# Kernel optimization log

Measured on AMD Instinct MI355X. Metric: run time of the kernel, lower is better.

## Reference

```python
import jax, jax.numpy as jnp
import numpy as np

# ---- module config (matches init_kwargs) ----
OGFH, OGFW = 256, 704
DOWNSAMPLE = 8
FH, FW = OGFH // DOWNSAMPLE, OGFW // DOWNSAMPLE   # 32, 88
DBOUND = (4.0, 45.0, 1.0)
D = int((DBOUND[1] - DBOUND[0]) / DBOUND[2])      # 41 depth bins
CAMC = 64
XB = (-50.0, 50.0, 0.5)    # lateral  -> nx = 200
YB = (-10.0, 10.0, 20.0)   # vertical -> ny = 1
ZB = (0.0, 50.0, 0.25)     # depth    -> nz = 200
NX = np.array([int((b[1] - b[0]) / b[2]) for b in (XB, YB, ZB)])  # [200, 1, 200]
DX = np.array([b[2] for b in (XB, YB, ZB)], dtype=np.float32)
BX = np.array([b[0] + b[2] / 2.0 for b in (XB, YB, ZB)], dtype=np.float32)


def make_frustum():
    # matches create_frustum_1camera: [D, fH, fW, 3] of (u, v, depth)
    ds = jnp.broadcast_to(
        jnp.arange(DBOUND[0], DBOUND[1], DBOUND[2], dtype=jnp.float32)[:, None, None],
        (D, FH, FW))
    xs = jnp.broadcast_to(
        jnp.linspace(0.0, OGFW - 1, FW, dtype=jnp.float32)[None, None, :], (D, FH, FW))
    ys = jnp.broadcast_to(
        jnp.linspace(0.0, OGFH - 1, FH, dtype=jnp.float32)[None, :, None], (D, FH, FW))
    return jnp.stack((xs, ys, ds), -1)


def setup_inputs() -> dict:
    key = jax.random.key(0)
    B = 4
    # depthnet output: first D channels = depth logits, next CAMC = context feats
    x = jax.random.normal(key, (B, D + CAMC, FH, FW), dtype=jnp.float32)
    fx = fy = 520.0
    K = jnp.array([[fx, 0.0, OGFW / 2.0],
                   [0.0, fy, OGFH / 2.0],
                   [0.0, 0.0, 1.0]], dtype=jnp.float32)
    intrins = jnp.broadcast_to(K, (B, 3, 3))
    post_rots = jnp.broadcast_to(jnp.eye(3, dtype=jnp.float32), (B, 3, 3))
    post_trans = jnp.zeros((B, 3), dtype=jnp.float32)
    return {"x": x, "intrins": intrins, "post_rots": post_rots, "post_trans": post_trans}


def _forward(x, intrins, post_rots, post_trans):
    B = x.shape[0]
    frustum = make_frustum()                                                     # [D,H,W,3]
    # ---- get_geometry ----
    pts = frustum[None] - post_trans[:, None, None, None, :]                     # [B,D,H,W,3]
    pts = jnp.einsum('bij,bdhwj->bdhwi', jnp.linalg.inv(post_rots), pts)
    pts = jnp.concatenate([pts[..., :2] * pts[..., 2:3], pts[..., 2:3]], -1)     # un-normalize
    geom = jnp.einsum('bij,bdhwj->bdhwi', jnp.linalg.inv(intrins), pts)          # [B,D,H,W,3]
    # ---- lift: depth softmax (x) context features ----
    depth = jax.nn.softmax(x[:, :D], axis=1)                                     # [B,D,H,W]
    feat = x[:, D:D + CAMC]                                                      # [B,C,H,W]
    vol = depth[:, None] * feat[:, :, None]                                      # [B,C,D,H,W]
    vol = jnp.transpose(vol, (0, 2, 3, 4, 1))                                    # [B,D,H,W,C]
    # ---- voxel_splat (sort+cumsum trick == segmented sum) ----
    Nprime = B * D * FH * FW
    feats = vol.reshape(Nprime, CAMC)
    # torch .long() truncates toward zero -> astype(int32)
    coords = ((geom - (BX - DX / 2.0)) / DX).astype(jnp.int32).reshape(Nprime, 3)
    bix = jnp.repeat(jnp.arange(B, dtype=jnp.int32), Nprime // B)
    kept = ((coords[:, 0] >= 0) & (coords[:, 0] < int(NX[0])) &
            (coords[:, 1] >= 0) & (coords[:, 1] < int(NX[1])) &
            (coords[:, 2] >= 0) & (coords[:, 2] < int(NX[2])))
    nseg = int(NX[0] * NX[1] * NX[2]) * B
    ranks = (coords[:, 0] * (int(NX[1]) * int(NX[2]) * B)
             + coords[:, 1] * (int(NX[2]) * B)
             + coords[:, 2] * B + bix)
    ranks = jnp.where(kept, ranks, nseg)  # dump bucket for dropped points
    pooled = jax.ops.segment_sum(jnp.where(kept[:, None], feats, 0.0), ranks,
                                 num_segments=nseg + 1)[:nseg]
    final = pooled.reshape(int(NX[0]), int(NX[1]), int(NX[2]), B, CAMC)          # [x,y,z,B,C]
    final = jnp.transpose(final, (3, 4, 1, 2, 0))                                # [B,C,ny,nz,nx]
    # torch.cat(final.unbind(dim=2), 1): collapse ny into channels (y-major)
    final = jnp.transpose(final, (0, 2, 1, 3, 4)).reshape(
        B, CAMC * int(NX[1]), int(NX[2]), int(NX[0]))                            # [B,C,200,200]
    return final


def reference(x, intrins, post_rots, post_trans):
    return _forward(x, intrins, post_rots, post_trans)
```

## Files before the change

kernel.cpp:

```cpp
#include <hip/hip_runtime.h>
#include <math.h>

#define DD   41
#define FHh  32
#define FWw  88
#define CC   64
#define CH   32
#define CG8  8
#define NXx  200
#define NZz  200
#define NCH  (DD + CC)
#define PLANE ((size_t)FHh * FWw)
#define NE   (DD * FWw)
#define DCAP 4
#define OVCAP 4096

__global__ __launch_bounds__(256) void lss_colpool(
    const float* __restrict__ x,
    const float* __restrict__ intrins,
    const float* __restrict__ post_rots,
    const float* __restrict__ post_trans,
    float* __restrict__ P, int* __restrict__ V,
    int* __restrict__ rowcnt8, int* __restrict__ ovcnt,
    float* __restrict__ out, int out_quads)
{
    __shared__ float Wt[DD][FHh + 1];
    __shared__ float F4s[FHh][36];
    __shared__ float Mi[18];
    __shared__ float pm[8][FHh + 1];
    __shared__ int   Vtmp[DD];

    int blk   = blockIdx.x;
    int chalf = blk & 1;
    int w     = (blk >> 1) % FWw;
    int b     = blk / (2 * FWw);
    int t     = threadIdx.x;
    const float* xb = x + (size_t)b * NCH * PLANE + w;

    for (int idx = t; idx < DD * FHh; idx += 256) {
        int d = idx >> 5, h = idx & 31;
        Wt[d][h] = xb[((size_t)d * FHh + h) * FWw];
    }
    for (int idx = t; idx < FHh * CH; idx += 256) {
        int c = idx & 31, h = idx >> 5;
        F4s[h][c] = xb[((size_t)(DD + chalf * CH + c) * FHh + h) * FWw];
    }
    if (t >= 64 && t < 64 + DD) Vtmp[t - 64] = -1;
    if (t == 0) {
        #pragma clang fp contract(off)
        for (int m = 0; m < 2; ++m) {
            const float* A = (m == 0 ? post_rots : intrins) + b * 9;
            float* O = Mi + m * 9;
            float a = A[0], bb = A[1], c = A[2];
            float d = A[3], e  = A[4], f = A[5];
            float g = A[6], h  = A[7], i = A[8];
            float det = a * (e * i - f * h) - bb * (d * i - f * g) + c * (d * h - e * g);
            O[0] = (e * i - f * h) / det;
            O[1] = (c * h - bb * i) / det;
            O[2] = (bb * f - c * e) / det;
            O[3] = (f * g - d * i) / det;
            O[4] = (a * i - c * g) / det;
            O[5] = (c * d - a * f) / det;
            O[6] = (d * h - e * g) / det;
            O[7] = (bb * g - a * h) / det;
            O[8] = (a * e - bb * d) / det;
        }
    }
    __syncthreads();

    int h = t & 31, l = t >> 5;
    float e_[6];
    {
        float pmax = -INFINITY;
        for (int d = l; d < DD; d += 8) pmax = fmaxf(pmax, Wt[d][h]);
        pm[l][h] = pmax;
    }
    __syncthreads();
    float mx = -INFINITY;
    for (int j = 0; j < 8; ++j) mx = fmaxf(mx, pm[j][h]);
    __syncthreads();
    {
        #pragma clang fp contract(off)
        float psum = 0.0f;
        int k = 0;
        for (int d = l; d < DD; d += 8, ++k) {
            float e = expf(Wt[d][h] - mx);
            e_[k] = e; psum += e;
        }
        pm[l][h] = psum;
    }
    __syncthreads();
    float s = 0.0f;
    for (int j = 0; j < 8; ++j) s += pm[j][h];

    {
        #pragma clang fp contract(off)
        float xs = (float)((double)w * 703.0 / 87.0);
        float ys = (float)((double)h * 255.0 / 31.0);
        float tx = post_trans[b * 3 + 0];
        float ty = post_trans[b * 3 + 1];
        float tz = post_trans[b * 3 + 2];
        int k = 0;
        for (int d = l; d < DD; d += 8, ++k) {
            float z  = 4.0f + (float)d;
            float px = xs - tx, py = ys - ty, pz = z - tz;
            float rx = Mi[0] * px + Mi[1] * py + Mi[2] * pz;
            float ry = Mi[3] * px + Mi[4] * py + Mi[5] * pz;
            float rz = Mi[6] * px + Mi[7] * py + Mi[8] * pz;
            float qx = rx * rz, qy = ry * rz, qz = rz;
            float gx = Mi[ 9] * qx + Mi[10] * qy + Mi[11] * qz;
            float gy = Mi[12] * qx + Mi[13] * qy + Mi[14] * qz;
            float gz = Mi[15] * qx + Mi[16] * qy + Mi[17] * qz;
            float cx = (gx + 50.0f) / 0.5f;
            float cy = (gy + 10.0f) / 20.0f;
            float cz = gz / 0.25f;
            int ix = (int)cx;
            int iy = (int)cy;
            int iz = (int)cz;
            bool kept = (ix >= 0) & (ix < NXx) & (iy == 0) & (iz >= 0) & (iz < NZz);
            if (kept) {
                Wt[d][h] = e_[k] / s;
                Vtmp[d] = iz * NXx + ix;
            } else {
                Wt[d][h] = 0.0f;
            }
        }
    }
    __syncthreads();

    float* Pb = P + ((size_t)b * NE) * CC + chalf * CH;
    {
        int c4 = t & 7;
        for (int d = t >> 3; d < DD; d += 32) {
            float4 acc = make_float4(0.f, 0.f, 0.f, 0.f);
            for (int hh = 0; hh < FHh; ++hh) {
                float wtv = Wt[d][hh];
                float4 fv = *(const float4*)&F4s[hh][c4 * 4];
                acc.x += wtv * fv.x; acc.y += wtv * fv.y;
                acc.z += wtv * fv.z; acc.w += wtv * fv.w;
            }
            *(float4*)&Pb[((size_t)d * FWw + w) * CC + c4 * 4] = acc;
        }
    }
    if (chalf == 0) {
        if (t < DD) V[(size_t)b * NE + (size_t)t * FWw + w] = Vtmp[t];
        if (w == 0) for (int i = t; i < NZz * 8; i += 256) rowcnt8[b * NZz * 8 + i] = 0;
    }
    if (blk == 0 && t == 0) *ovcnt = 0;

    {
        float4 z = make_float4(0.f, 0.f, 0.f, 0.f);
        float4* o4 = (float4*)out;
        int stride = gridDim.x * 256;
        for (int i = blk * 256 + t; i < out_quads; i += stride) o4[i] = z;
    }
}

__global__ __launch_bounds__(256) void lss_rowbuild(
    const float* __restrict__ P, const int* __restrict__ V,
    float* __restrict__ S, int* __restrict__ izd,
    int* __restrict__ rowcnt8, int* __restrict__ dlist8,
    int* __restrict__ ovcnt, int* __restrict__ ovlist,
    float* __restrict__ out)
{
    __shared__ float acc[CG8 * (NXx + 1)];
    __shared__ int ixw[FWw];
    __shared__ int izw[FWw];
    __shared__ int key;
    __shared__ int s_k;

    int blk = blockIdx.x;
    int cg = blk & 7;
    int bd = blk >> 3;
    int d = bd % DD;
    int b = bd / DD;
    int t = threadIdx.x;

    if (t == 0) key = 0x7fffffff;
    for (int i = t; i < CG8 * (NXx + 1); i += 256) acc[i] = 0.0f;
    __syncthreads();
    if (t < FWw) {
        int v = V[(size_t)bd * FWw + t];
        if (v >= 0) {
            int iz = v / NXx;
            izw[t] = iz; ixw[t] = v - iz * NXx;
            atomicMin(&key, (t << 16) | iz);
        } else { izw[t] = -1; ixw[t] = -1; }
    }
    __syncthreads();
    int kk = key;
    int s_iz = (kk == 0x7fffffff) ? -1 : (kk & 0xffff);
    if (cg == 0 && t == 0) izd[bd] = s_iz;
    if (s_iz < 0) return;

    int r = b * NZz + s_iz;
    if (t == 0) {
        int k = atomicAdd(&rowcnt8[r * 8 + cg], 1);
        if (k < DCAP) dlist8[(r * 8 + cg) * DCAP + k] = d;
        s_k = k;
    }
    if (cg == 0 && t < FWw && izw[t] >= 0 && izw[t] != s_iz) {
        int k = atomicAdd(ovcnt, 1);
        if (k < OVCAP)
            ovlist[k] = (b << 29) | (d << 23) | (t << 16) | (ixw[t] << 8) | izw[t];
    }

    const float* Pb = P + (size_t)bd * FWw * CC + cg * CG8;
    for (int idx = t; idx < FWw * 2; idx += 256) {
        int w = idx >> 1, q = idx & 1;
        if (izw[w] == s_iz) {
            float4 v = *(const float4*)&Pb[(size_t)w * CC + q * 4];
            int ix = ixw[w];
            int cb = q * 4;
            atomicAdd(&acc[(cb + 0) * (NXx + 1) + ix], v.x);
            atomicAdd(&acc[(cb + 1) * (NXx + 1) + ix], v.y);
            atomicAdd(&acc[(cb + 2) * (NXx + 1) + ix], v.z);
            atomicAdd(&acc[(cb + 3) * (NXx + 1) + ix], v.w);
        }
    }
    __syncthreads();

    bool owner0 = (s_k == 0);
    for (int i = t; i < CG8 * (NXx / 4); i += 256) {
        int c = i / (NXx / 4), q = i - c * (NXx / 4);
        int base = c * (NXx + 1) + q * 4;
        float4 vv;
        vv.x = acc[base + 0];
        vv.y = acc[base + 1];
        vv.z = acc[base + 2];
        vv.w = acc[base + 3];
        if (owner0) {
            float* orow = out + (((size_t)(b * CC + cg * CG8 + c)) * NZz + s_iz) * NXx;
            ((float4*)orow)[q] = vv;
        } else {
            float* Srow = S + ((size_t)bd * CC + cg * CG8 + c) * NXx;
            ((float4*)Srow)[q] = vv;
        }
    }
}

__global__ __launch_bounds__(256) void lss_fixup(
    const float* __restrict__ S, const int* __restrict__ izd,
    const int* __restrict__ rowcnt8, const int* __restrict__ dlist8,
    const float* __restrict__ P,
    const int* __restrict__ ovcnt, const int* __restrict__ ovlist,
    float* __restrict__ out)
{
    int b = blockIdx.x;
    int t = threadIdx.x;

    for (int pair = t; pair < NZz * 8; pair += 256) {
        int n = rowcnt8[b * NZz * 8 + pair];
        if (n <= 1) continue;
        int iz = pair >> 3, cg = pair & 7;
        const int* dl = dlist8 + (size_t)(b * NZz * 8 + pair) * DCAP;
        if (n <= DCAP) {
            for (int k = 1; k < n; ++k) {
                int d = dl[k];
                for (int c = 0; c < CG8; ++c) {
                    const float* Srow = S + ((size_t)(b * DD + d) * CC + cg * CG8 + c) * NXx;
                    float* orow = out + (((size_t)(b * CC + cg * CG8 + c)) * NZz + iz) * NXx;
                    for (int ix = 0; ix < NXx; ++ix) atomicAdd(&orow[ix], Srow[ix]);
                }
            }
        } else {
            int owner0 = dl[0];
            for (int d = 0; d < DD; ++d) {
                if (izd[b * DD + d] == iz && d != owner0) {
                    for (int c = 0; c < CG8; ++c) {
                        const float* Srow = S + ((size_t)(b * DD + d) * CC + cg * CG8 + c) * NXx;
                        float* orow = out + (((size_t)(b * CC + cg * CG8 + c)) * NZz + iz) * NXx;
                        for (int ix = 0; ix < NXx; ++ix) atomicAdd(&orow[ix], Srow[ix]);
                    }
                }
            }
        }
    }

    if (b == 0 && t == 0) {
        int nov = *ovcnt;
        if (nov > OVCAP) nov = OVCAP;
        for (int k = 0; k < nov; ++k) {
            int ent = ovlist[k];
            int eb  = (ent >> 29) & 7;
            int ed  = (ent >> 23) & 63;
            int ew  = (ent >> 16) & 127;
            int eix = (ent >> 8) & 255;
            int eiz = ent & 255;
            for (int c = 0; c < CC; ++c) {
                size_t o = (((size_t)(eb * CC + c)) * NZz + eiz) * NXx + eix;
                atomicAdd(&out[o], P[(((size_t)eb * DD + ed) * FWw + ew) * CC + c]);
            }
        }
    }
}

extern "C" void kernel_launch(void* const* d_in, const int* in_sizes, int n_in,
                              void* d_out, int out_size, void* d_ws, size_t ws_size,
                              hipStream_t stream)
{
    const float* x          = (const float*)d_in[0];
    const float* intrins    = (const float*)d_in[1];
    const float* post_rots  = (const float*)d_in[2];
    const float* post_trans = (const float*)d_in[3];
    float* out = (float*)d_out;

    int B = in_sizes[0] / (NCH * (int)PLANE);

    size_t off = 0;
    auto alloc = [&](size_t bytes) {
        void* p = (char*)d_ws + off;
        off = (off + bytes + 255) & ~(size_t)255;
        return p;
    };
    float* P       = (float*)alloc((size_t)B * NE * CC * sizeof(float));
    int*   V       = (int*)  alloc((size_t)B * NE * sizeof(int));
    float* S       = (float*)alloc((size_t)B * DD * CC * NXx * sizeof(float));
    int*   izd     = (int*)  alloc((size_t)B * DD * sizeof(int));
    int*   rowcnt8 = (int*)  alloc((size_t)B * NZz * 8 * sizeof(int));
    int*   dlist8  = (int*)  alloc((size_t)B * NZz * 8 * DCAP * sizeof(int));
    int*   ovcnt   = (int*)  alloc(256);
    int*   ovlist  = (int*)  alloc((size_t)OVCAP * sizeof(int));

    int out_quads = out_size / 4;

    lss_colpool<<<B * FWw * 2, 256, 0, stream>>>(x, intrins, post_rots, post_trans,
                                                 P, V, rowcnt8, ovcnt, out, out_quads);
    lss_rowbuild<<<B * DD * 8, 256, 0, stream>>>(P, V, S, izd, rowcnt8, dlist8,
                                                 ovcnt, ovlist, out);
    lss_fixup<<<B, 256, 0, stream>>>(S, izd, rowcnt8, dlist8, P, ovcnt, ovlist, out);
}
```

Baseline: 99.60 us.

## Fuse column pooling into depth splat, precompute softmax stats in prep kernel

```diff
diff --git a/kernel.cpp b/kernel.cpp
--- a/kernel.cpp
+++ b/kernel.cpp
@@ -5,167 +5,107 @@
 #define FHh  32
 #define FWw  88
 #define CC   64
-#define CH   32
 #define CG8  8
 #define NXx  200
 #define NZz  200
 #define NCH  (DD + CC)
-#define PLANE ((size_t)FHh * FWw)
-#define NE   (DD * FWw)
+#define PLANE 2816
 #define DCAP 4
 #define OVCAP 4096
 
-__global__ __launch_bounds__(256) void lss_colpool(
+__device__ __forceinline__ void inv3x3_pair(const float* __restrict__ intrins,
+                                            const float* __restrict__ post_rots,
+                                            int b, float* O18)
+{
+    #pragma clang fp contract(off)
+    for (int m = 0; m < 2; ++m) {
+        const float* A = (m == 0 ? post_rots : intrins) + b * 9;
+        float* O = O18 + m * 9;
+        float a = A[0], bb = A[1], c = A[2];
+        float d = A[3], e  = A[4], f = A[5];
+        float g = A[6], h  = A[7], i = A[8];
+        float det = a * (e * i - f * h) - bb * (d * i - f * g) + c * (d * h - e * g);
+        O[0] = (e * i - f * h) / det;
+        O[1] = (c * h - bb * i) / det;
+        O[2] = (bb * f - c * e) / det;
+        O[3] = (f * g - d * i) / det;
+        O[4] = (a * i - c * g) / det;
+        O[5] = (c * d - a * f) / det;
+        O[6] = (d * h - e * g) / det;
+        O[7] = (bb * g - a * h) / det;
+        O[8] = (a * e - bb * d) / det;
+    }
+}
+
+__device__ __forceinline__ bool geom_point(const float* __restrict__ Mi,
+                                           float tx, float ty, float tz,
+                                           int d, int h, int w,
+                                           int* pix_, int* piz_)
+{
+    #pragma clang fp contract(off)
+    float xs = (float)((double)w * 703.0 / 87.0);
+    float ys = (float)((double)h * 255.0 / 31.0);
+    float z  = 4.0f + (float)d;
+    float px = xs - tx, py = ys - ty, pz = z - tz;
+    float rx = Mi[0] * px + Mi[1] * py + Mi[2] * pz;
+    float ry = Mi[3] * px + Mi[4] * py + Mi[5] * pz;
+    float rz = Mi[6] * px + Mi[7] * py + Mi[8] * pz;
+    float qx = rx * rz, qy = ry * rz, qz = rz;
+    float gx = Mi[ 9] * qx + Mi[10] * qy + Mi[11] * qz;
+    float gy = Mi[12] * qx + Mi[13] * qy + Mi[14] * qz;
+    float gz = Mi[15] * qx + Mi[16] * qy + Mi[17] * qz;
+    float cx = (gx + 50.0f) / 0.5f;
+    float cy = (gy + 10.0f) / 20.0f;
+    float cz = gz / 0.25f;
+    int ix = (int)cx;
+    int iy = (int)cy;
+    int iz = (int)cz;
+    *pix_ = ix; *piz_ = iz;
+    return (ix >= 0) & (ix < NXx) & (iy == 0) & (iz >= 0) & (iz < NZz);
+}
+
+__global__ __launch_bounds__(256) void lss_prep(
+    const float* __restrict__ x, float* __restrict__ m, float* __restrict__ s,
+    int* __restrict__ rowcnt8, int* __restrict__ ovcnt,
+    float* __restrict__ out, int out_quads, int B)
+{
+    int gid = blockIdx.x * 256 + threadIdx.x;
+    int stride = gridDim.x * 256;
+
+    int npix = B * PLANE;
+    for (int pix = gid; pix < npix; pix += stride) {
+        int b = pix / PLANE, p = pix - b * PLANE;
+        const float* xp = x + (size_t)b * NCH * PLANE + p;
+        float mm = -INFINITY;
+        for (int d = 0; d < DD; ++d) mm = fmaxf(mm, xp[(size_t)d * PLANE]);
+        float ss = 0.0f;
+        for (int d = 0; d < DD; ++d) ss += expf(xp[(size_t)d * PLANE] - mm);
+        m[pix] = mm; s[pix] = ss;
+    }
+
+    for (int i = gid; i < B * NZz * 8; i += stride) rowcnt8[i] = 0;
+    if (gid == 0) *ovcnt = 0;
+
+    float4 z = make_float4(0.f, 0.f, 0.f, 0.f);
+    float4* o4 = (float4*)out;
+    for (int i = gid; i < out_quads; i += stride) o4[i] = z;
+}
+
+__global__ __launch_bounds__(256) void lss_dsplat(
     const float* __restrict__ x,
+    const float* __restrict__ m, const float* __restrict__ s,
     const float* __restrict__ intrins,
     const float* __restrict__ post_rots,
     const float* __restrict__ post_trans,
-    float* __restrict__ P, int* __restrict__ V,
-    int* __restrict__ rowcnt8, int* __restrict__ ovcnt,
-    float* __restrict__ out, int out_quads)
-{
-    __shared__ float Wt[DD][FHh + 1];
-    __shared__ float F4s[FHh][36];
-    __shared__ float Mi[18];
-    __shared__ float pm[8][FHh + 1];
-    __shared__ int   Vtmp[DD];
-
-    int blk   = blockIdx.x;
-    int chalf = blk & 1;
-    int w     = (blk >> 1) % FWw;
-    int b     = blk / (2 * FWw);
-    int t     = threadIdx.x;
-    const float* xb = x + (size_t)b * NCH * PLANE + w;
-
-    for (int idx = t; idx < DD * FHh; idx += 256) {
-        int d = idx >> 5, h = idx & 31;
-        Wt[d][h] = xb[((size_t)d * FHh + h) * FWw];
-    }
-    for (int idx = t; idx < FHh * CH; idx += 256) {
-        int c = idx & 31, h = idx >> 5;
-        F4s[h][c] = xb[((size_t)(DD + chalf * CH + c) * FHh + h) * FWw];
-    }
-    if (t >= 64 && t < 64 + DD) Vtmp[t - 64] = -1;
-    if (t == 0) {
-        #pragma clang fp contract(off)
-        for (int m = 0; m < 2; ++m) {
-            const float* A = (m == 0 ? post_rots : intrins) + b * 9;
-            float* O = Mi + m * 9;
-            float a = A[0], bb = A[1], c = A[2];
-            float d = A[3], e  = A[4], f = A[5];
-            float g = A[6], h  = A[7], i = A[8];
-            float det = a * (e * i - f * h) - bb * (d * i - f * g) + c * (d * h - e * g);
-            O[0] = (e * i - f * h) / det;
-            O[1] = (c * h - bb * i) / det;
-            O[2] = (bb * f - c * e) / det;
-            O[3] = (f * g - d * i) / det;
-            O[4] = (a * i - c * g) / det;
-            O[5] = (c * d - a * f) / det;
-            O[6] = (d * h - e * g) / det;
-            O[7] = (bb * g - a * h) / det;
-            O[8] = (a * e - bb * d) / det;
-        }
-    }
-    __syncthreads();
-
-    int h = t & 31, l = t >> 5;
-    float e_[6];
-    {
-        float pmax = -INFINITY;
-        for (int d = l; d < DD; d += 8) pmax = fmaxf(pmax, Wt[d][h]);
-        pm[l][h] = pmax;
-    }
-    __syncthreads();
-    float mx = -INFINITY;
-    for (int j = 0; j < 8; ++j) mx = fmaxf(mx, pm[j][h]);
-    __syncthreads();
-    {
-        #pragma clang fp contract(off)
-        float psum = 0.0f;
-        int k = 0;
-        for (int d = l; d < DD; d += 8, ++k) {
-            float e = expf(Wt[d][h] - mx);
-            e_[k] = e; psum += e;
-        }
-        pm[l][h] = psum;
-    }
-    __syncthreads();
-    float s = 0.0f;
-    for (int j = 0; j < 8; ++j) s += pm[j][h];
-
-    {
-        #pragma clang fp contract(off)
-        float xs = (float)((double)w * 703.0 / 87.0);
-        float ys = (float)((double)h * 255.0 / 31.0);
-        float tx = post_trans[b * 3 + 0];
-        float ty = post_trans[b * 3 + 1];
-        float tz = post_trans[b * 3 + 2];
-        int k = 0;
-        for (int d = l; d < DD; d += 8, ++k) {
-            float z  = 4.0f + (float)d;
-            float px = xs - tx, py = ys - ty, pz = z - tz;
-            float rx = Mi[0] * px + Mi[1] * py + Mi[2] * pz;
-            float ry = Mi[3] * px + Mi[4] * py + Mi[5] * pz;
-            float rz = Mi[6] * px + Mi[7] * py + Mi[8] * pz;
-            float qx = rx * rz, qy = ry * rz, qz = rz;
-            float gx = Mi[ 9] * qx + Mi[10] * qy + Mi[11] * qz;
-            float gy = Mi[12] * qx + Mi[13] * qy + Mi[14] * qz;
-            float gz = Mi[15] * qx + Mi[16] * qy + Mi[17] * qz;
-            float cx = (gx + 50.0f) / 0.5f;
-            float cy = (gy + 10.0f) / 20.0f;
-            float cz = gz / 0.25f;
-            int ix = (int)cx;
-            int iy = (int)cy;
-            int iz = (int)cz;
-            bool kept = (ix >= 0) & (ix < NXx) & (iy == 0) & (iz >= 0) & (iz < NZz);
-            if (kept) {
-                Wt[d][h] = e_[k] / s;
-                Vtmp[d] = iz * NXx + ix;
-            } else {
-                Wt[d][h] = 0.0f;
-            }
-        }
-    }
-    __syncthreads();
-
-    float* Pb = P + ((size_t)b * NE) * CC + chalf * CH;
-    {
-        int c4 = t & 7;
-        for (int d = t >> 3; d < DD; d += 32) {
-            float4 acc = make_float4(0.f, 0.f, 0.f, 0.f);
-            for (int hh = 0; hh < FHh; ++hh) {
-                float wtv = Wt[d][hh];
-                float4 fv = *(const float4*)&F4s[hh][c4 * 4];
-                acc.x += wtv * fv.x; acc.y += wtv * fv.y;
-                acc.z += wtv * fv.z; acc.w += wtv * fv.w;
-            }
-            *(float4*)&Pb[((size_t)d * FWw + w) * CC + c4 * 4] = acc;
-        }
-    }
-    if (chalf == 0) {
-        if (t < DD) V[(size_t)b * NE + (size_t)t * FWw + w] = Vtmp[t];
-        if (w == 0) for (int i = t; i < NZz * 8; i += 256) rowcnt8[b * NZz * 8 + i] = 0;
-    }
-    if (blk == 0 && t == 0) *ovcnt = 0;
-
-    {
-        float4 z = make_float4(0.f, 0.f, 0.f, 0.f);
-        float4* o4 = (float4*)out;
-        int stride = gridDim.x * 256;
-        for (int i = blk * 256 + t; i < out_quads; i += stride) o4[i] = z;
-    }
-}
-
-__global__ __launch_bounds__(256) void lss_rowbuild(
-    const float* __restrict__ P, const int* __restrict__ V,
     float* __restrict__ S, int* __restrict__ izd,
     int* __restrict__ rowcnt8, int* __restrict__ dlist8,
     int* __restrict__ ovcnt, int* __restrict__ ovlist,
     float* __restrict__ out)
 {
+    __shared__ float Wt[PLANE];
     __shared__ float acc[CG8 * (NXx + 1)];
-    __shared__ int ixw[FWw];
-    __shared__ int izw[FWw];
+    __shared__ float Mi[18];
+    __shared__ int ixw[FWw], izw[FWw];
     __shared__ int key;
     __shared__ int s_k;
 
@@ -176,22 +116,41 @@
     int b = bd / DD;
     int t = threadIdx.x;
 
-    if (t == 0) key = 0x7fffffff;
+    if (t == 0) { key = 0x7fffffff; inv3x3_pair(intrins, post_rots, b, Mi); }
+    if (t < FWw) { ixw[t] = -1; izw[t] = -1; }
     for (int i = t; i < CG8 * (NXx + 1); i += 256) acc[i] = 0.0f;
     __syncthreads();
-    if (t < FWw) {
-        int v = V[(size_t)bd * FWw + t];
-        if (v >= 0) {
-            int iz = v / NXx;
-            izw[t] = iz; ixw[t] = v - iz * NXx;
-            atomicMin(&key, (t << 16) | iz);
-        } else { izw[t] = -1; ixw[t] = -1; }
+
+    float tx = post_trans[b * 3 + 0];
+    float ty = post_trans[b * 3 + 1];
+    float tz = post_trans[b * 3 + 2];
+
+    const float* xb = x + (size_t)b * NCH * PLANE;
+    for (int p = t; p < PLANE; p += 256) {
+        int h = p / FWw, w = p - h * FWw;
+        float logit = xb[(size_t)d * PLANE + p];
+        int ix, iz;
+        bool kept = geom_point(Mi, tx, ty, tz, d, h, w, &ix, &iz);
+        float wt = 0.0f;
+        if (kept) {
+            int pix = b * PLANE + p;
+            wt = expf(logit - m[pix]) / s[pix];
+            ixw[w] = ix; izw[w] = iz;
+            atomicMin(&key, (w << 16) | iz);
+        }
+        Wt[p] = wt;
     }
     __syncthreads();
+
     int kk = key;
     int s_iz = (kk == 0x7fffffff) ? -1 : (kk & 0xffff);
     if (cg == 0 && t == 0) izd[bd] = s_iz;
     if (s_iz < 0) return;
+
+    if (cg == 0 && t < FWw && izw[t] >= 0 && izw[t] != s_iz) {
+        int k = atomicAdd(ovcnt, 1);
+        if (k < OVCAP) ovlist[k] = (b << 16) | (d << 8) | t;
+    }
 
     int r = b * NZz + s_iz;
     if (t == 0) {
@@ -199,24 +158,16 @@
         if (k < DCAP) dlist8[(r * 8 + cg) * DCAP + k] = d;
         s_k = k;
     }
-    if (cg == 0 && t < FWw && izw[t] >= 0 && izw[t] != s_iz) {
-        int k = atomicAdd(ovcnt, 1);
-        if (k < OVCAP)
-            ovlist[k] = (b << 29) | (d << 23) | (t << 16) | (ixw[t] << 8) | izw[t];
-    }
-
-    const float* Pb = P + (size_t)bd * FWw * CC + cg * CG8;
-    for (int idx = t; idx < FWw * 2; idx += 256) {
-        int w = idx >> 1, q = idx & 1;
-        if (izw[w] == s_iz) {
-            float4 v = *(const float4*)&Pb[(size_t)w * CC + q * 4];
-            int ix = ixw[w];
-            int cb = q * 4;
-            atomicAdd(&acc[(cb + 0) * (NXx + 1) + ix], v.x);
-            atomicAdd(&acc[(cb + 1) * (NXx + 1) + ix], v.y);
-            atomicAdd(&acc[(cb + 2) * (NXx + 1) + ix], v.z);
-            atomicAdd(&acc[(cb + 3) * (NXx + 1) + ix], v.w);
-        }
+
+    const float* Fb = xb + (size_t)(DD + cg * CG8) * PLANE;
+    for (int pair = t; pair < CG8 * FWw; pair += 256) {
+        int c = pair / FWw, w = pair - c * FWw;
+        if (izw[w] != s_iz) continue;
+        const float* Fc = Fb + (size_t)c * PLANE + w;
+        float a = 0.0f;
+        #pragma unroll 8
+        for (int h = 0; h < FHh; ++h) a += Wt[h * FWw + w] * Fc[(size_t)h * FWw];
+        atomicAdd(&acc[c * (NXx + 1) + ixw[w]], a);
     }
     __syncthreads();
 
@@ -240,9 +191,13 @@
 }
 
 __global__ __launch_bounds__(256) void lss_fixup(
+    const float* __restrict__ x,
+    const float* __restrict__ m, const float* __restrict__ s,
+    const float* __restrict__ intrins,
+    const float* __restrict__ post_rots,
+    const float* __restrict__ post_trans,
     const float* __restrict__ S, const int* __restrict__ izd,
     const int* __restrict__ rowcnt8, const int* __restrict__ dlist8,
-    const float* __restrict__ P,
     const int* __restrict__ ovcnt, const int* __restrict__ ovlist,
     float* __restrict__ out)
 {
@@ -254,19 +209,21 @@
         if (n <= 1) continue;
         int iz = pair >> 3, cg = pair & 7;
         const int* dl = dlist8 + (size_t)(b * NZz * 8 + pair) * DCAP;
-        if (n <= DCAP) {
-            for (int k = 1; k < n; ++k) {
-                int d = dl[k];
-                for (int c = 0; c < CG8; ++c) {
-                    const float* Srow = S + ((size_t)(b * DD + d) * CC + cg * CG8 + c) * NXx;
-                    float* orow = out + (((size_t)(b * CC + cg * CG8 + c)) * NZz + iz) * NXx;
-                    for (int ix = 0; ix < NXx; ++ix) atomicAdd(&orow[ix], Srow[ix]);
-                }
+        int nn = (n <= DCAP) ? n : DCAP;
+        for (int k = 1; k < nn; ++k) {
+            int d = dl[k];
+            for (int c = 0; c < CG8; ++c) {
+                const float* Srow = S + ((size_t)(b * DD + d) * CC + cg * CG8 + c) * NXx;
+                float* orow = out + (((size_t)(b * CC + cg * CG8 + c)) * NZz + iz) * NXx;
+                for (int ix = 0; ix < NXx; ++ix) atomicAdd(&orow[ix], Srow[ix]);
             }
-        } else {
+        }
+        if (n > DCAP) {
             int owner0 = dl[0];
             for (int d = 0; d < DD; ++d) {
-                if (izd[b * DD + d] == iz && d != owner0) {
+                bool indl = false;
+                for (int k = 0; k < nn; ++k) indl |= (dl[k] == d);
+                if (izd[b * DD + d] == iz && d != owner0 && !indl) {
                     for (int c = 0; c < CG8; ++c) {
                         const float* Srow = S + ((size_t)(b * DD + d) * CC + cg * CG8 + c) * NXx;
                         float* orow = out + (((size_t)(b * CC + cg * CG8 + c)) * NZz + iz) * NXx;
@@ -280,16 +237,27 @@
     if (b == 0 && t == 0) {
         int nov = *ovcnt;
         if (nov > OVCAP) nov = OVCAP;
+        float Mi[18];
         for (int k = 0; k < nov; ++k) {
             int ent = ovlist[k];
-            int eb  = (ent >> 29) & 7;
-            int ed  = (ent >> 23) & 63;
-            int ew  = (ent >> 16) & 127;
-            int eix = (ent >> 8) & 255;
-            int eiz = ent & 255;
-            for (int c = 0; c < CC; ++c) {
-                size_t o = (((size_t)(eb * CC + c)) * NZz + eiz) * NXx + eix;
-                atomicAdd(&out[o], P[(((size_t)eb * DD + ed) * FWw + ew) * CC + c]);
+            int eb = (ent >> 16) & 0x7f;
+            int ed = (ent >> 8) & 0xff;
+            int ew = ent & 0xff;
+            inv3x3_pair(intrins, post_rots, eb, Mi);
+            float tx = post_trans[eb * 3 + 0];
+            float ty = post_trans[eb * 3 + 1];
+            float tz = post_trans[eb * 3 + 2];
+            const float* xb = x + (size_t)eb * NCH * PLANE;
+            for (int h = 0; h < FHh; ++h) {
+                int ix, iz;
+                if (!geom_point(Mi, tx, ty, tz, ed, h, ew, &ix, &iz)) continue;
+                int p = h * FWw + ew;
+                int pix = eb * PLANE + p;
+                float wt = expf(xb[(size_t)ed * PLANE + p] - m[pix]) / s[pix];
+                for (int c = 0; c < CC; ++c) {
+                    size_t o = (((size_t)(eb * CC + c)) * NZz + iz) * NXx + ix;
+                    atomicAdd(&out[o], wt * xb[(size_t)(DD + c) * PLANE + p]);
+                }
             }
         }
     }
@@ -305,7 +273,7 @@
     const float* post_trans = (const float*)d_in[3];
     float* out = (float*)d_out;
 
-    int B = in_sizes[0] / (NCH * (int)PLANE);
+    int B = in_sizes[0] / (NCH * PLANE);
 
     size_t off = 0;
     auto alloc = [&](size_t bytes) {
@@ -313,8 +281,8 @@
         off = (off + bytes + 255) & ~(size_t)255;
         return p;
     };
-    float* P       = (float*)alloc((size_t)B * NE * CC * sizeof(float));
-    int*   V       = (int*)  alloc((size_t)B * NE * sizeof(int));
+    float* m       = (float*)alloc((size_t)B * PLANE * sizeof(float));
+    float* s       = (float*)alloc((size_t)B * PLANE * sizeof(float));
     float* S       = (float*)alloc((size_t)B * DD * CC * NXx * sizeof(float));
     int*   izd     = (int*)  alloc((size_t)B * DD * sizeof(int));
     int*   rowcnt8 = (int*)  alloc((size_t)B * NZz * 8 * sizeof(int));
@@ -324,9 +292,9 @@
 
     int out_quads = out_size / 4;
 
-    lss_colpool<<<B * FWw * 2, 256, 0, stream>>>(x, intrins, post_rots, post_trans,
-                                                 P, V, rowcnt8, ovcnt, out, out_quads);
-    lss_rowbuild<<<B * DD * 8, 256, 0, stream>>>(P, V, S, izd, rowcnt8, dlist8,
-                                                 ovcnt, ovlist, out);
-    lss_fixup<<<B, 256, 0, stream>>>(S, izd, rowcnt8, dlist8, P, ovcnt, ovlist, out);
-}
+    lss_prep<<<1024, 256, 0, stream>>>(x, m, s, rowcnt8, ovcnt, out, out_quads, B);
+    lss_dsplat<<<B * DD * 8, 256, 0, stream>>>(x, m, s, intrins, post_rots, post_trans,
+                                               S, izd, rowcnt8, dlist8, ovcnt, ovlist, out);
+    lss_fixup<<<B, 256, 0, stream>>>(x, m, s, intrins, post_rots, post_trans,
+                                     S, izd, rowcnt8, dlist8, ovcnt, ovlist, out);
+}
```

Result: slower. 146.1 us (+46.7%).

## Fuse three kernels into one persistent launch with atomic inter-block barriers

Applied to the files above, without the earlier changes.

```diff
diff --git a/kernel.cpp b/kernel.cpp
--- a/kernel.cpp
+++ b/kernel.cpp
@@ -15,22 +15,31 @@
 #define DCAP 4
 #define OVCAP 4096
 
-__global__ __launch_bounds__(256) void lss_colpool(
+struct ColShm {
+    float Wt[DD][FHh + 1];
+    float F4s[FHh][36];
+    float Mi[18];
+    float pm[8][FHh + 1];
+    int   Vtmp[DD];
+};
+struct RowShm {
+    float acc[CG8 * (NXx + 1)];
+    int   ixw[FWw];
+    int   izw[FWw];
+    int   key;
+    int   s_k;
+};
+union Shm { ColShm c; RowShm r; };
+
+__device__ void dev_colpool(int blk, int NA, ColShm& S,
     const float* __restrict__ x,
     const float* __restrict__ intrins,
     const float* __restrict__ post_rots,
     const float* __restrict__ post_trans,
     float* __restrict__ P, int* __restrict__ V,
-    int* __restrict__ rowcnt8, int* __restrict__ ovcnt,
+    int* __restrict__ rowcnt8,
     float* __restrict__ out, int out_quads)
 {
-    __shared__ float Wt[DD][FHh + 1];
-    __shared__ float F4s[FHh][36];
-    __shared__ float Mi[18];
-    __shared__ float pm[8][FHh + 1];
-    __shared__ int   Vtmp[DD];
-
-    int blk   = blockIdx.x;
     int chalf = blk & 1;
     int w     = (blk >> 1) % FWw;
     int b     = blk / (2 * FWw);
@@ -39,18 +48,18 @@
 
     for (int idx = t; idx < DD * FHh; idx += 256) {
         int d = idx >> 5, h = idx & 31;
-        Wt[d][h] = xb[((size_t)d * FHh + h) * FWw];
+        S.Wt[d][h] = xb[((size_t)d * FHh + h) * FWw];
     }
     for (int idx = t; idx < FHh * CH; idx += 256) {
         int c = idx & 31, h = idx >> 5;
-        F4s[h][c] = xb[((size_t)(DD + chalf * CH + c) * FHh + h) * FWw];
-    }
-    if (t >= 64 && t < 64 + DD) Vtmp[t - 64] = -1;
+        S.F4s[h][c] = xb[((size_t)(DD + chalf * CH + c) * FHh + h) * FWw];
+    }
+    if (t >= 64 && t < 64 + DD) S.Vtmp[t - 64] = -1;
     if (t == 0) {
         #pragma clang fp contract(off)
         for (int m = 0; m < 2; ++m) {
             const float* A = (m == 0 ? post_rots : intrins) + b * 9;
-            float* O = Mi + m * 9;
+            float* O = S.Mi + m * 9;
             float a = A[0], bb = A[1], c = A[2];
             float d = A[3], e  = A[4], f = A[5];
             float g = A[6], h  = A[7], i = A[8];
@@ -72,26 +81,26 @@
     float e_[6];
     {
         float pmax = -INFINITY;
-        for (int d = l; d < DD; d += 8) pmax = fmaxf(pmax, Wt[d][h]);
-        pm[l][h] = pmax;
+        for (int d = l; d < DD; d += 8) pmax = fmaxf(pmax, S.Wt[d][h]);
+        S.pm[l][h] = pmax;
     }
     __syncthreads();
     float mx = -INFINITY;
-    for (int j = 0; j < 8; ++j) mx = fmaxf(mx, pm[j][h]);
+    for (int j = 0; j < 8; ++j) mx = fmaxf(mx, S.pm[j][h]);
     __syncthreads();
     {
         #pragma clang fp contract(off)
         float psum = 0.0f;
         int k = 0;
         for (int d = l; d < DD; d += 8, ++k) {
-            float e = expf(Wt[d][h] - mx);
+            float e = expf(S.Wt[d][h] - mx);
             e_[k] = e; psum += e;
         }
-        pm[l][h] = psum;
+        S.pm[l][h] = psum;
     }
     __syncthreads();
     float s = 0.0f;
-    for (int j = 0; j < 8; ++j) s += pm[j][h];
+    for (int j = 0; j < 8; ++j) s += S.pm[j][h];
 
     {
         #pragma clang fp contract(off)
@@ -104,13 +113,13 @@
         for (int d = l; d < DD; d += 8, ++k) {
             float z  = 4.0f + (float)d;
             float px = xs - tx, py = ys - ty, pz = z - tz;
-            float rx = Mi[0] * px + Mi[1] * py + Mi[2] * pz;
-            float ry = Mi[3] * px + Mi[4] * py + Mi[5] * pz;
-            float rz = Mi[6] * px + Mi[7] * py + Mi[8] * pz;
+            float rx = S.Mi[0] * px + S.Mi[1] * py + S.Mi[2] * pz;
+            float ry = S.Mi[3] * px + S.Mi[4] * py + S.Mi[5] * pz;
+            float rz = S.Mi[6] * px + S.Mi[7] * py + S.Mi[8] * pz;
             float qx = rx * rz, qy = ry * rz, qz = rz;
-            float gx = Mi[ 9] * qx + Mi[10] * qy + Mi[11] * qz;
-            float gy = Mi[12] * qx + Mi[13] * qy + Mi[14] * qz;
-            float gz = Mi[15] * qx + Mi[16] * qy + Mi[17] * qz;
+            float gx = S.Mi[ 9] * qx + S.Mi[10] * qy + S.Mi[11] * qz;
+            float gy = S.Mi[12] * qx + S.Mi[13] * qy + S.Mi[14] * qz;
+            float gz = S.Mi[15] * qx + S.Mi[16] * qy + S.Mi[17] * qz;
             float cx = (gx + 50.0f) / 0.5f;
             float cy = (gy + 10.0f) / 20.0f;
             float cz = gz / 0.25f;
@@ -119,10 +128,10 @@
             int iz = (int)cz;
             bool kept = (ix >= 0) & (ix < NXx) & (iy == 0) & (iz >= 0) & (iz < NZz);
             if (kept) {
-                Wt[d][h] = e_[k] / s;
-                Vtmp[d] = iz * NXx + ix;
+                S.Wt[d][h] = e_[k] / s;
+                S.Vtmp[d] = iz * NXx + ix;
             } else {
-                Wt[d][h] = 0.0f;
+                S.Wt[d][h] = 0.0f;
             }
         }
     }
@@ -134,8 +143,8 @@
         for (int d = t >> 3; d < DD; d += 32) {
             float4 acc = make_float4(0.f, 0.f, 0.f, 0.f);
             for (int hh = 0; hh < FHh; ++hh) {
-                float wtv = Wt[d][hh];
-                float4 fv = *(const float4*)&F4s[hh][c4 * 4];
+                float wtv = S.Wt[d][hh];
+                float4 fv = *(const float4*)&S.F4s[hh][c4 * 4];
                 acc.x += wtv * fv.x; acc.y += wtv * fv.y;
                 acc.z += wtv * fv.z; acc.w += wtv * fv.w;
             }
@@ -143,52 +152,44 @@
         }
     }
     if (chalf == 0) {
-        if (t < DD) V[(size_t)b * NE + (size_t)t * FWw + w] = Vtmp[t];
+        if (t < DD) V[(size_t)b * NE + (size_t)t * FWw + w] = S.Vtmp[t];
         if (w == 0) for (int i = t; i < NZz * 8; i += 256) rowcnt8[b * NZz * 8 + i] = 0;
     }
-    if (blk == 0 && t == 0) *ovcnt = 0;
 
     {
         float4 z = make_float4(0.f, 0.f, 0.f, 0.f);
         float4* o4 = (float4*)out;
-        int stride = gridDim.x * 256;
+        int stride = NA * 256;
         for (int i = blk * 256 + t; i < out_quads; i += stride) o4[i] = z;
     }
 }
 
-__global__ __launch_bounds__(256) void lss_rowbuild(
+__device__ void dev_rowbuild(int blk, RowShm& S,
     const float* __restrict__ P, const int* __restrict__ V,
-    float* __restrict__ S, int* __restrict__ izd,
+    float* __restrict__ Spark, int* __restrict__ izd,
     int* __restrict__ rowcnt8, int* __restrict__ dlist8,
     int* __restrict__ ovcnt, int* __restrict__ ovlist,
     float* __restrict__ out)
 {
-    __shared__ float acc[CG8 * (NXx + 1)];
-    __shared__ int ixw[FWw];
-    __shared__ int izw[FWw];
-    __shared__ int key;
-    __shared__ int s_k;
-
-    int blk = blockIdx.x;
     int cg = blk & 7;
     int bd = blk >> 3;
     int d = bd % DD;
     int b = bd / DD;
     int t = threadIdx.x;
 
-    if (t == 0) key = 0x7fffffff;
-    for (int i = t; i < CG8 * (NXx + 1); i += 256) acc[i] = 0.0f;
+    if (t == 0) S.key = 0x7fffffff;
+    for (int i = t; i < CG8 * (NXx + 1); i += 256) S.acc[i] = 0.0f;
     __syncthreads();
     if (t < FWw) {
         int v = V[(size_t)bd * FWw + t];
         if (v >= 0) {
             int iz = v / NXx;
-            izw[t] = iz; ixw[t] = v - iz * NXx;
-            atomicMin(&key, (t << 16) | iz);
-        } else { izw[t] = -1; ixw[t] = -1; }
-    }
-    __syncthreads();
-    int kk = key;
+            S.izw[t] = iz; S.ixw[t] = v - iz * NXx;
+            atomicMin(&S.key, (t << 16) | iz);
+        } else { S.izw[t] = -1; S.ixw[t] = -1; }
+    }
+    __syncthreads();
+    int kk = S.key;
     int s_iz = (kk == 0x7fffffff) ? -1 : (kk & 0xffff);
     if (cg == 0 && t == 0) izd[bd] = s_iz;
     if (s_iz < 0) return;
@@ -197,87 +198,88 @@
     if (t == 0) {
         int k = atomicAdd(&rowcnt8[r * 8 + cg], 1);
         if (k < DCAP) dlist8[(r * 8 + cg) * DCAP + k] = d;
-        s_k = k;
-    }
-    if (cg == 0 && t < FWw && izw[t] >= 0 && izw[t] != s_iz) {
+        S.s_k = k;
+    }
+    if (cg == 0 && t < FWw && S.izw[t] >= 0 && S.izw[t] != s_iz) {
         int k = atomicAdd(ovcnt, 1);
         if (k < OVCAP)
-            ovlist[k] = (b << 29) | (d << 23) | (t << 16) | (ixw[t] << 8) | izw[t];
+            ovlist[k] = (b << 29) | (d << 23) | (t << 16) | (S.ixw[t] << 8) | S.izw[t];
     }
 
     const float* Pb = P + (size_t)bd * FWw * CC + cg * CG8;
     for (int idx = t; idx < FWw * 2; idx += 256) {
         int w = idx >> 1, q = idx & 1;
-        if (izw[w] == s_iz) {
+        if (S.izw[w] == s_iz) {
             float4 v = *(const float4*)&Pb[(size_t)w * CC + q * 4];
-            int ix = ixw[w];
+            int ix = S.ixw[w];
             int cb = q * 4;
-            atomicAdd(&acc[(cb + 0) * (NXx + 1) + ix], v.x);
-            atomicAdd(&acc[(cb + 1) * (NXx + 1) + ix], v.y);
-            atomicAdd(&acc[(cb + 2) * (NXx + 1) + ix], v.z);
-            atomicAdd(&acc[(cb + 3) * (NXx + 1) + ix], v.w);
-        }
-    }
-    __syncthreads();
-
-    bool owner0 = (s_k == 0);
+            atomicAdd(&S.acc[(cb + 0) * (NXx + 1) + ix], v.x);
+            atomicAdd(&S.acc[(cb + 1) * (NXx + 1) + ix], v.y);
+            atomicAdd(&S.acc[(cb + 2) * (NXx + 1) + ix], v.z);
+            atomicAdd(&S.acc[(cb + 3) * (NXx + 1) + ix], v.w);
+        }
+    }
+    __syncthreads();
+
+    bool owner0 = (S.s_k == 0);
     for (int i = t; i < CG8 * (NXx / 4); i += 256) {
         int c = i / (NXx / 4), q = i - c * (NXx / 4);
         int base = c * (NXx + 1) + q * 4;
         float4 vv;
-        vv.x = acc[base + 0];
-        vv.y = acc[base + 1];
-        vv.z = acc[base + 2];
-        vv.w = acc[base + 3];
+        vv.x = S.acc[base + 0];
+        vv.y = S.acc[base + 1];
+        vv.z = S.acc[base + 2];
+        vv.w = S.acc[base + 3];
         if (owner0) {
             float* orow = out + (((size_t)(b * CC + cg * CG8 + c)) * NZz + s_iz) * NXx;
             ((float4*)orow)[q] = vv;
         } else {
-            float* Srow = S + ((size_t)bd * CC + cg * CG8 + c) * NXx;
+            float* Srow = Spark + ((size_t)bd * CC + cg * CG8 + c) * NXx;
             ((float4*)Srow)[q] = vv;
         }
     }
 }
 
-__global__ __launch_bounds__(256) void lss_fixup(
-    const float* __restrict__ S, const int* __restrict__ izd,
+__device__ void dev_fixup(int B,
+    const float* __restrict__ Spark, const int* __restrict__ izd,
     const int* __restrict__ rowcnt8, const int* __restrict__ dlist8,
     const float* __restrict__ P,
     const int* __restrict__ ovcnt, const int* __restrict__ ovlist,
     float* __restrict__ out)
 {
-    int b = blockIdx.x;
     int t = threadIdx.x;
-
-    for (int pair = t; pair < NZz * 8; pair += 256) {
-        int n = rowcnt8[b * NZz * 8 + pair];
-        if (n <= 1) continue;
-        int iz = pair >> 3, cg = pair & 7;
-        const int* dl = dlist8 + (size_t)(b * NZz * 8 + pair) * DCAP;
-        if (n <= DCAP) {
-            for (int k = 1; k < n; ++k) {
+    for (int b = 0; b < B; ++b) {
+        for (int pair = t; pair < NZz * 8; pair += 256) {
+            int n = rowcnt8[b * NZz * 8 + pair];
+            if (n <= 1) continue;
+            int iz = pair >> 3, cg = pair & 7;
+            const int* dl = dlist8 + (size_t)(b * NZz * 8 + pair) * DCAP;
+            int nn = (n <= DCAP) ? n : DCAP;
+            for (int k = 1; k < nn; ++k) {
                 int d = dl[k];
                 for (int c = 0; c < CG8; ++c) {
-                    const float* Srow = S + ((size_t)(b * DD + d) * CC + cg * CG8 + c) * NXx;
+                    const float* Srow = Spark + ((size_t)(b * DD + d) * CC + cg * CG8 + c) * NXx;
                     float* orow = out + (((size_t)(b * CC + cg * CG8 + c)) * NZz + iz) * NXx;
                     for (int ix = 0; ix < NXx; ++ix) atomicAdd(&orow[ix], Srow[ix]);
                 }
             }
-        } else {
-            int owner0 = dl[0];
-            for (int d = 0; d < DD; ++d) {
-                if (izd[b * DD + d] == iz && d != owner0) {
-                    for (int c = 0; c < CG8; ++c) {
-                        const float* Srow = S + ((size_t)(b * DD + d) * CC + cg * CG8 + c) * NXx;
-                        float* orow = out + (((size_t)(b * CC + cg * CG8 + c)) * NZz + iz) * NXx;
-                        for (int ix = 0; ix < NXx; ++ix) atomicAdd(&orow[ix], Srow[ix]);
+            if (n > DCAP) {
+                int owner0 = dl[0];
+                for (int d = 0; d < DD; ++d) {
+                    bool indl = false;
+                    for (int k = 0; k < nn; ++k) indl |= (dl[k] == d);
+                    if (izd[b * DD + d] == iz && d != owner0 && !indl) {
+                        for (int c = 0; c < CG8; ++c) {
+                            const float* Srow = Spark + ((size_t)(b * DD + d) * CC + cg * CG8 + c) * NXx;
+                            float* orow = out + (((size_t)(b * CC + cg * CG8 + c)) * NZz + iz) * NXx;
+                            for (int ix = 0; ix < NXx; ++ix) atomicAdd(&orow[ix], Srow[ix]);
+                        }
                     }
                 }
             }
         }
     }
-
-    if (b == 0 && t == 0) {
+    if (t == 0) {
         int nov = *ovcnt;
         if (nov > OVCAP) nov = OVCAP;
         for (int k = 0; k < nov; ++k) {
@@ -295,6 +297,87 @@
     }
 }
 
+__global__ __launch_bounds__(256, 8) void lss_fused(
+    const float* __restrict__ x,
+    const float* __restrict__ intrins,
+    const float* __restrict__ post_rots,
+    const float* __restrict__ post_trans,
+    float* __restrict__ P, int* __restrict__ V,
+    float* __restrict__ Spark, int* __restrict__ izd,
+    int* __restrict__ rowcnt8, int* __restrict__ dlist8,
+    int* __restrict__ ctrl, int* __restrict__ ovlist,
+    float* __restrict__ out, int out_quads, int NA, int NB, int B)
+{
+    __shared__ Shm shm;
+    __shared__ int lastflag;
+    int bid = blockIdx.x;
+    int t = threadIdx.x;
+    int* done  = ctrl + 0;
+    int* done2 = ctrl + 16;
+    int* ovcnt = ctrl + 32;
+
+    if (bid < NA) {
+        dev_colpool(bid, NA, shm.c, x, intrins, post_rots, post_trans,
+                    P, V, rowcnt8, out, out_quads);
+        __syncthreads();
+        __threadfence();
+        if (t == 0)
+            __hip_atomic_fetch_add(done, 1, __ATOMIC_RELEASE, __HIP_MEMORY_SCOPE_AGENT);
+    } else {
+        if (t == 0) {
+            while (__hip_atomic_load(done, __ATOMIC_ACQUIRE, __HIP_MEMORY_SCOPE_AGENT) < NA)
+                __builtin_amdgcn_s_sleep(32);
+        }
+        __syncthreads();
+        dev_rowbuild(bid - NA, shm.r, P, V, Spark, izd, rowcnt8, dlist8,
+                     ovcnt, ovlist, out);
+        __syncthreads();
+        __threadfence();
+        if (t == 0) {
+            int k = __hip_atomic_fetch_add(done2, 1, __ATOMIC_ACQ_REL, __HIP_MEMORY_SCOPE_AGENT);
+            lastflag = (k == NB - 1) ? 1 : 0;
+        }
+        __syncthreads();
+        if (lastflag)
+            dev_fixup(B, Spark, izd, rowcnt8, dlist8, P, ovcnt, ovlist, out);
+    }
+}
+
+__global__ __launch_bounds__(256) void k_colpool(
+    const float* __restrict__ x, const float* __restrict__ intrins,
+    const float* __restrict__ post_rots, const float* __restrict__ post_trans,
+    float* __restrict__ P, int* __restrict__ V, int* __restrict__ rowcnt8,
+    float* __restrict__ out, int out_quads)
+{
+    __shared__ ColShm shm;
+    dev_colpool(blockIdx.x, gridDim.x, shm, x, intrins, post_rots, post_trans,
+                P, V, rowcnt8, out, out_quads);
+}
+
+__global__ __launch_bounds__(256) void k_rowfix(
+    const float* __restrict__ P, const int* __restrict__ V,
+    float* __restrict__ Spark, int* __restrict__ izd,
+    int* __restrict__ rowcnt8, int* __restrict__ dlist8,
+    int* __restrict__ ctrl, int* __restrict__ ovlist,
+    float* __restrict__ out, int B)
+{
+    __shared__ RowShm shm;
+    __shared__ int lastflag;
+    int t = threadIdx.x;
+    int* done2 = ctrl + 16;
+    int* ovcnt = ctrl + 32;
+    dev_rowbuild(blockIdx.x, shm, P, V, Spark, izd, rowcnt8, dlist8, ovcnt, ovlist, out);
+    __syncthreads();
+    __threadfence();
+    if (t == 0) {
+        int k = __hip_atomic_fetch_add(done2, 1, __ATOMIC_ACQ_REL, __HIP_MEMORY_SCOPE_AGENT);
+        lastflag = (k == (int)gridDim.x - 1) ? 1 : 0;
+    }
+    __syncthreads();
+    if (lastflag)
+        dev_fixup(B, Spark, izd, rowcnt8, dlist8, P, ovcnt, ovlist, out);
+}
+
 extern "C" void kernel_launch(void* const* d_in, const int* in_sizes, int n_in,
                               void* d_out, int out_size, void* d_ws, size_t ws_size,
                               hipStream_t stream)
@@ -315,18 +398,27 @@
     };
     float* P       = (float*)alloc((size_t)B * NE * CC * sizeof(float));
     int*   V       = (int*)  alloc((size_t)B * NE * sizeof(int));
-    float* S       = (float*)alloc((size_t)B * DD * CC * NXx * sizeof(float));
+    float* Spark   = (float*)alloc((size_t)B * DD * CC * NXx * sizeof(float));
     int*   izd     = (int*)  alloc((size_t)B * DD * sizeof(int));
     int*   rowcnt8 = (int*)  alloc((size_t)B * NZz * 8 * sizeof(int));
     int*   dlist8  = (int*)  alloc((size_t)B * NZz * 8 * DCAP * sizeof(int));
-    int*   ovcnt   = (int*)  alloc(256);
+    int*   ctrl    = (int*)  alloc(256);
     int*   ovlist  = (int*)  alloc((size_t)OVCAP * sizeof(int));
 
     int out_quads = out_size / 4;
-
-    lss_colpool<<<B * FWw * 2, 256, 0, stream>>>(x, intrins, post_rots, post_trans,
-                                                 P, V, rowcnt8, ovcnt, out, out_quads);
-    lss_rowbuild<<<B * DD * 8, 256, 0, stream>>>(P, V, S, izd, rowcnt8, dlist8,
-                                                 ovcnt, ovlist, out);
-    lss_fixup<<<B, 256, 0, stream>>>(S, izd, rowcnt8, dlist8, P, ovcnt, ovlist, out);
-}
+    int NA = B * FWw * 2;
+    int NB = B * DD * 8;
+
+    (void)hipMemsetAsync(ctrl, 0, 256, stream);
+
+    if (NA + NB <= 2048) {
+        lss_fused<<<NA + NB, 256, 0, stream>>>(x, intrins, post_rots, post_trans,
+                                               P, V, Spark, izd, rowcnt8, dlist8,
+                                               ctrl, ovlist, out, out_quads, NA, NB, B);
+    } else {
+        k_colpool<<<NA, 256, 0, stream>>>(x, intrins, post_rots, post_trans,
+                                          P, V, rowcnt8, out, out_quads);
+        k_rowfix<<<NB, 256, 0, stream>>>(P, V, Spark, izd, rowcnt8, dlist8,
+                                         ctrl, ovlist, out, B);
+    }
+}
```

Result: slower. 352.2 us (+253.6%).
